# Optimization experiments

Hardware: AMD Instinct MI355X
Metric: run time of the kernel (lower is better)

The kernel has to match this reference:

```python
import jax, jax.numpy as jnp
import numpy as np

M = 256      # num memories in bnn_history
D = 7686     # input_size (2 agent one-hot + 7680 embedding + 4 scalars)
H = 256      # NEAT hidden nodes
O = 4        # NEAT output nodes
N = D + H + O  # total nodes in dense weight matrix


def setup_inputs() -> dict:
    key = jax.random.key(0)
    ks = jax.random.split(key, 8)
    inv_sqrt_d = 1.0 / np.sqrt(D).astype(np.float32)
    return {
        "input_matrix": jax.random.normal(ks[0], (M, D), jnp.float32),
        "Wq": jax.random.normal(ks[1], (D, D), jnp.float32) * inv_sqrt_d,
        "bq": jnp.zeros((D,), jnp.float32),
        "Wk": jax.random.normal(ks[2], (D, D), jnp.float32) * inv_sqrt_d,
        "bk": jnp.zeros((D,), jnp.float32),
        "Wv": jax.random.normal(ks[3], (D, D), jnp.float32) * inv_sqrt_d,
        "bv": jnp.zeros((D,), jnp.float32),
        "weight_mu": jax.random.normal(ks[4], (N, N), jnp.float32) * 0.01,
        "weight_sigma": jnp.full((N, N), 0.1, jnp.float32),  # build_network inits sigma to 0.1
        "bias_mu": jnp.zeros((H + O,), jnp.float32),
        "bias_sigma": jnp.full((H + O,), 0.1, jnp.float32),
        "eps_w": jax.random.normal(ks[5], (N, N), jnp.float32),
        "eps_b": jax.random.normal(ks[6], (H + O,), jnp.float32),
    }


def reference(input_matrix, Wq, bq, Wk, bk, Wv, bv,
              weight_mu, weight_sigma, bias_mu, bias_sigma, eps_w, eps_b):
    # --- attention over memory rows (nn.Linear applies x @ W.T + b) ---
    Q = input_matrix @ Wq.T + bq            # [M, D]
    K = input_matrix @ Wk.T + bk            # [M, D]
    V = input_matrix @ Wv.T + bv            # [M, D]
    scale = 1.0 / jnp.sqrt(jnp.asarray(D, input_matrix.dtype))
    attn = jax.nn.softmax((Q @ K.T) * scale, axis=-1)  # [M, M]
    context = (attn @ V).mean(axis=0)       # [D] pooled attended context

    # --- Bayesian reparameterized genome weights / biases ---
    W = weight_mu + weight_sigma * eps_w    # [N, N], W[i, j] = weight of edge i->j
    b = bias_mu + bias_sigma * eps_b        # [H+O]

    # --- topological NEAT-style evaluation: inputs, then hidden, then outputs ---
    values0 = jnp.zeros((N,), input_matrix.dtype).at[:D].set(context)

    def step(values, j):
        col = jax.lax.dynamic_slice_in_dim(W, j, 1, axis=1)[:, 0]  # incoming weights of node j
        pre = values @ col + b[j - D]        # sum aggregation + bias
        return values.at[j].set(jnp.tanh(pre)), None

    values, _ = jax.lax.scan(step, values0, jnp.arange(D, N))
    return values[-O:]                       # output node activations
```

## Files before the change

### kernel.cpp

```cpp
#include <hip/hip_runtime.h>
#include <hip/hip_bf16.h>
#include <type_traits>

#define DIN   7686
#define NNODE 7946
#define HOUT  260
#define KP    8192

typedef __attribute__((ext_vector_type(8))) short bf16x8;
typedef __attribute__((ext_vector_type(4))) float f32x4;

__device__ __forceinline__ unsigned int f2b(float f) {
  union { float f; unsigned int u; } v; v.f = f;
  return (v.u + 0x7FFFu + ((v.u >> 16) & 1u)) >> 16;
}
__device__ __forceinline__ unsigned int pack2(float lo, float hi) {
  unsigned int r;
  asm("v_cvt_pk_bf16_f32 %0, %1, %2" : "=v"(r) : "v"(lo), "v"(hi));
  return r;
}
__device__ __forceinline__ float b2f(unsigned short h) {
  union { unsigned int u; float f; } v; v.u = ((unsigned int)h) << 16; return v.f;
}
__device__ __forceinline__ void gload16(const void* g, void* l) {
  __builtin_amdgcn_global_load_lds(
      (const __attribute__((address_space(1))) unsigned int*)g,
      (__attribute__((address_space(3))) unsigned int*)l, 16, 0, 0);
}
__device__ __forceinline__ float readlane_f(float v, int lane) {
  return __uint_as_float(__builtin_amdgcn_readlane(__float_as_uint(v), lane));
}

__global__ void prep_x(const float* __restrict__ X, unsigned short* __restrict__ XbT)
{
  const int m = blockIdx.x, t = threadIdx.x;
  const float* row = X + (size_t)m * DIN;
#pragma unroll
  for (int c2 = 0; c2 < 4; ++c2) {
    const int k8 = (c2 * 256 + t) * 8;
    float f[8];
    if (k8 + 8 <= DIN) {
#pragma unroll
      for (int h = 0; h < 4; ++h) {
        float2 v = *(const float2*)(row + k8 + h * 2);
        f[h * 2] = v.x; f[h * 2 + 1] = v.y;
      }
    } else {
#pragma unroll
      for (int h = 0; h < 8; ++h) f[h] = (k8 + h < DIN) ? row[k8 + h] : 0.f;
    }
    uint4 o;
    o.x = pack2(f[0], f[1]); o.y = pack2(f[2], f[3]);
    o.z = pack2(f[4], f[5]); o.w = pack2(f[6], f[7]);
    const int kc = k8 >> 7;
    char* dst = (char*)XbT + (size_t)kc * 65536 + m * 256 +
                (((k8 & 127) * 2) ^ ((m & 7) << 4));
    *(uint4*)dst = o;
  }
}

__global__ __launch_bounds__(512)
void gemm_qk2(const unsigned short* __restrict__ XbT,
              const float* __restrict__ Wq, const float* __restrict__ Wk,
              const float* __restrict__ bq, const float* __restrict__ bk,
              unsigned short* __restrict__ Qbf, unsigned short* __restrict__ Kbf)
{
  const int mat = blockIdx.y;
  const float* W = mat ? Wk : Wq;
  const float* bias = mat ? bk : bq;
  unsigned short* Out = mat ? Kbf : Qbf;
  const int nt = blockIdx.x, n0 = nt * 64;
  const int tid = threadIdx.x, l = tid & 63, wv = tid >> 6;
  const int wr = wv >> 1, wc = wv & 1;
  const int lm = l & 15;

  __shared__ __align__(16) unsigned short As[2][32768];
  __shared__ __align__(16) unsigned short Bs[8192];

  long long wrb[8];
#pragma unroll
  for (int r = 0; r < 8; ++r) {
    int rg = n0 + wv * 8 + r;
    if (rg > DIN - 1) rg = DIN - 1;
    wrb[r] = (long long)rg * DIN;
  }

  float2 breg[8];
  auto RLOADB = [&](int s) {
    const int ss = (s < 64) ? s : 63;
    const int kk = ss * 128 + l * 2;
    const int kcl = (kk < DIN) ? kk : 0;
    const bool ok = kk < DIN;
#pragma unroll
    for (int r = 0; r < 8; ++r) {
      float2 v = *(const float2*)(W + wrb[r] + kcl);
      if (!ok) { v.x = 0.f; v.y = 0.f; }
      breg[r] = v;
    }
  };
  auto SWRITE = [&]() {
#pragma unroll
    for (int r = 0; r < 8; ++r) {
      const int lrow = wv * 8 + r;
      const int off = lrow * 256 + ((l * 4) ^ ((r & 7) << 4));
      *(unsigned int*)((char*)Bs + off) = pack2(breg[r].x, breg[r].y);
    }
  };
  auto GLOADA = [&](int s, int buf) {
    const int kc = (s < 64) ? s : 63;
    const char* g = (const char*)XbT + (size_t)kc * 65536;
    char* lb = (char*)&As[buf][0];
#pragma unroll
    for (int q = 0; q < 8; ++q) {
      const int chunk = q * 8 + wv;
      gload16(g + chunk * 1024 + l * 16, lb + chunk * 1024);
    }
  };

  f32x4 acc[4][2] = {};
  const int sw = (l & 7) << 4;
  const int lq16 = ((l >> 4) & 3) * 16;

  auto COMPUTE = [&](int buf) {
    const char* a_ = (const char*)&As[buf][0];
    const char* b_ = (const char*)Bs;
#pragma unroll
    for (int ks = 0; ks < 4; ++ks) {
      bf16x8 bf[2];
#pragma unroll
      for (int j = 0; j < 2; ++j) {
        const int n = wc * 32 + j * 16 + lm;
        bf[j] = *(const bf16x8*)(b_ + n * 256 + ((ks * 64 + lq16) ^ sw));
      }
#pragma unroll
      for (int i = 0; i < 4; ++i) {
        const int m = wr * 64 + i * 16 + lm;
        bf16x8 a = *(const bf16x8*)(a_ + m * 256 + ((ks * 64 + lq16) ^ sw));
        acc[i][0] = __builtin_amdgcn_mfma_f32_16x16x32_bf16(a, bf[0], acc[i][0], 0, 0, 0);
        acc[i][1] = __builtin_amdgcn_mfma_f32_16x16x32_bf16(a, bf[1], acc[i][1], 0, 0, 0);
      }
    }
  };

#define WAITV(n) { asm volatile("s_waitcnt vmcnt(" #n ")" ::: "memory"); \
                   __builtin_amdgcn_sched_barrier(0); }
#define WAITL    { asm volatile("s_waitcnt lgkmcnt(0)" ::: "memory"); \
                   __builtin_amdgcn_sched_barrier(0); }

  RLOADB(0); GLOADA(0, 0);
  WAITV(0)
  SWRITE();
  RLOADB(1); GLOADA(1, 1);
  WAITL
  __builtin_amdgcn_s_barrier();

  for (int s = 0; s < 64; ++s) {
    COMPUTE(s & 1);
    if (s == 63) break;
    WAITV(8)
    __builtin_amdgcn_s_barrier();
    SWRITE();
    RLOADB(s + 2);
    GLOADA(s + 2, s & 1);
    WAITL
    WAITV(16)
    __builtin_amdgcn_s_barrier();
  }
#undef WAITV
#undef WAITL

#pragma unroll
  for (int i = 0; i < 4; ++i) {
    const int r0 = wr * 64 + i * 16 + (l >> 4) * 4;
#pragma unroll
    for (int j = 0; j < 2; ++j) {
      const int col = n0 + wc * 32 + j * 16 + lm;
      const float bb = (col < DIN) ? bias[col] : 0.f;
#pragma unroll
      for (int q = 0; q < 4; ++q) {
        const float v = acc[i][j][q] + bb;
        Out[(size_t)(r0 + q) * KP + col] = (col < DIN) ? (unsigned short)f2b(v) : 0;
      }
    }
  }
}

__global__ __launch_bounds__(512)
void gemm_logits(const unsigned short* __restrict__ Qbf,
                 const unsigned short* __restrict__ Kbf, float* __restrict__ LP)
{
  const int qr = blockIdx.x & 1, qc = blockIdx.x >> 1, z = blockIdx.z;
  const int tid = threadIdx.x, lane = tid & 63, wv = tid >> 6;
  const int lm = lane & 15, lq = (lane >> 4) * 8;
  const int rowBase = qr * 128 + (wv & 3) * 32;
  const int colBase = qc * 128 + (wv >> 2) * 64;
  const int k0 = z * 128;
  f32x4 acc[2][4] = {};
#pragma unroll
  for (int ks = 0; ks < 4; ++ks) {
    bf16x8 a[2], b[4];
#pragma unroll
    for (int i = 0; i < 2; ++i)
      a[i] = *(const bf16x8*)(Qbf + (size_t)(rowBase + i * 16 + lm) * KP + k0 + ks * 32 + lq);
#pragma unroll
    for (int j = 0; j < 4; ++j)
      b[j] = *(const bf16x8*)(Kbf + (size_t)(colBase + j * 16 + lm) * KP + k0 + ks * 32 + lq);
#pragma unroll
    for (int i = 0; i < 2; ++i)
#pragma unroll
      for (int j = 0; j < 4; ++j)
        acc[i][j] = __builtin_amdgcn_mfma_f32_16x16x32_bf16(a[i], b[j], acc[i][j], 0, 0, 0);
  }
  float* out = LP + (size_t)z * 65536;
#pragma unroll
  for (int i = 0; i < 2; ++i) {
    const int r0 = rowBase + i * 16 + (lane >> 4) * 4;
#pragma unroll
    for (int j = 0; j < 4; ++j) {
      const int col = colBase + j * 16 + lm;
#pragma unroll
      for (int q = 0; q < 4; ++q)
        out[(size_t)(r0 + q) * 256 + col] = acc[i][j][q];
    }
  }
}

__global__ void softmax_fused(const float* __restrict__ LP, float* __restrict__ abar)
{
  __shared__ float red[8];
  const int m = blockIdx.x, t = threadIdx.x;
  float v = 0.f;
#pragma unroll 8
  for (int zz = 0; zz < 64; ++zz) v += LP[(size_t)zz * 65536 + m * 256 + t];
  const float scale = 1.0f / sqrtf((float)DIN);
  float mx = v;
#pragma unroll
  for (int o = 32; o >= 1; o >>= 1) mx = fmaxf(mx, __shfl_xor(mx, o, 64));
  if ((t & 63) == 0) red[t >> 6] = mx;
  __syncthreads();
  mx = fmaxf(fmaxf(red[0], red[1]), fmaxf(red[2], red[3]));
  float e = __expf((v - mx) * scale);
  float s = e;
#pragma unroll
  for (int o = 32; o >= 1; o >>= 1) s += __shfl_xor(s, o, 64);
  if ((t & 63) == 0) red[4 + (t >> 6)] = s;
  __syncthreads();
  s = red[4] + red[5] + red[6] + red[7];
  atomicAdd(&abar[t], e * (1.0f / 256.0f) / s);
}

__global__ void y_kernel(const float* __restrict__ X, const float* __restrict__ abar,
                         float* __restrict__ y)
{
  __shared__ float ab[256];
  ab[threadIdx.x] = abar[threadIdx.x];
  __syncthreads();
  const int c = blockIdx.x * 256 + threadIdx.x;
  if (c >= DIN) return;
  float s = 0.f;
#pragma unroll 8
  for (int m = 0; m < 256; ++m) s += ab[m] * X[(size_t)m * DIN + c];
  y[c] = s;
}

__global__ __launch_bounds__(512)
void ctx_mv(const float* __restrict__ Wv, const float* __restrict__ y,
            const float* __restrict__ bv, float* __restrict__ ctx)
{
  const int wv = threadIdx.x >> 6, l = threadIdx.x & 63;
  const int row = blockIdx.x * 8 + wv;
  if (row >= DIN) return;
  const float* wr_ = Wv + (size_t)row * DIN;
  float s = 0.f;
  for (int it = 0; it < 61; ++it) {
    const int k = it * 128 + l * 2;
    if (k < DIN) {
      float2 w2 = *(const float2*)(wr_ + k);
      float2 y2 = *(const float2*)(y + k);
      s = fmaf(w2.x, y2.x, s);
      s = fmaf(w2.y, y2.y, s);
    }
  }
#pragma unroll
  for (int o = 32; o >= 1; o >>= 1) s += __shfl_xor(s, o, 64);
  if (l == 0) ctx[row] = s + bv[row];
}

__global__ void base_kernel(const float* __restrict__ mu, const float* __restrict__ sg,
                            const float* __restrict__ ep, const float* __restrict__ ctx,
                            float* __restrict__ base)
{
  const int j = threadIdx.x;
  if (j >= HOUT) return;
  const int i0 = blockIdx.x * 31;
  const int i1 = min(i0 + 31, DIN);
  float acc = 0.f;
#pragma unroll 4
  for (int i = i0; i < i1; ++i) {
    const size_t idx = (size_t)i * NNODE + DIN + j;
    acc = fmaf(ctx[i], fmaf(sg[idx], ep[idx], mu[idx]), acc);
  }
  atomicAdd(&base[j], acc);
}

__global__ void ws_kernel(const float* __restrict__ mu, const float* __restrict__ sg,
                          const float* __restrict__ ep, float* __restrict__ WsG)
{
  const int t = blockIdx.x;
  const int j = threadIdx.x;
  if (j >= HOUT) return;
  const size_t idx = (size_t)(DIN + t) * NNODE + DIN + j;
  WsG[t * HOUT + j] = fmaf(sg[idx], ep[idx], mu[idx]);
}

__global__ __launch_bounds__(64, 1)
void scan2(const float* __restrict__ WsG, const float* __restrict__ base,
           const float* __restrict__ bmu, const float* __restrict__ bsg,
           const float* __restrict__ epb, float* __restrict__ out)
{
  __shared__ __align__(16) float tile[32 * HOUT + 128];
  const int l = threadIdx.x;

  float a0, a1, a2, a3, a4;
  {
    int j = l;       a0 = base[j] + bmu[j] + bsg[j] * epb[j];
    j = l + 64;      a1 = base[j] + bmu[j] + bsg[j] * epb[j];
    j = l + 128;     a2 = base[j] + bmu[j] + bsg[j] * epb[j];
    j = l + 192;     a3 = base[j] + bmu[j] + bsg[j] * epb[j];
    j = l + 256;     a4 = (j < HOUT) ? (base[j] + bmu[j] + bsg[j] * epb[j]) : 0.f;
  }

  float4 stg[33];
  auto LOADT = [&](int tb) {
    const int nfl = ((tb == 8) ? 4 : 32) * HOUT;
    const float* src = WsG + tb * 32 * HOUT;
#pragma unroll
    for (int c = 0; c < 33; ++c) {
      const int o = c * 256 + l * 4;
      if (o < nfl) stg[c] = *(const float4*)(src + o);
    }
  };
  auto WRITET = [&](int tb) {
    const int nfl = ((tb == 8) ? 4 : 32) * HOUT;
#pragma unroll
    for (int c = 0; c < 33; ++c) {
      const int o = c * 256 + l * 4;
      if (o < nfl) *(float4*)&tile[o] = stg[c];
    }
  };

  float w0, w1, w2, w3, w4;
  auto PRER = [&](int trow) {
    const float* tr = tile + trow * HOUT;
    w0 = tr[l]; w1 = tr[l + 64]; w2 = tr[l + 128]; w3 = tr[l + 192]; w4 = tr[l + 256];
  };

  auto inner = [&](auto Bc, int tb, int nrows) {
    constexpr int B = Bc.value;
    for (int tt = 0; tt < nrows; ++tt) {
      const int t = tb * 32 + tt;
      float pre;
      if constexpr (B == 0) pre = readlane_f(a0, t & 63);
      else if constexpr (B == 1) pre = readlane_f(a1, t & 63);
      else if constexpr (B == 2) pre = readlane_f(a2, t & 63);
      else if constexpr (B == 3) pre = readlane_f(a3, t & 63);
      else pre = readlane_f(a4, t & 63);
      const float pc = fminf(fmaxf(pre, -12.f), 12.f);
      const float e = __expf(2.f * pc);
      const float vt = 1.f - 2.f / (e + 1.f);
      if (t >= 256 && l == 0) out[t - 256] = vt;
      if (l > t)            a0 = fmaf(vt, w0, a0);
      if (l + 64 > t)       a1 = fmaf(vt, w1, a1);
      if (l + 128 > t)      a2 = fmaf(vt, w2, a2);
      if (l + 192 > t)      a3 = fmaf(vt, w3, a3);
      if (l + 256 > t && l + 256 < HOUT) a4 = fmaf(vt, w4, a4);
      if (tt + 1 < nrows) PRER(tt + 1);
    }
  };

  LOADT(0); WRITET(0); PRER(0);

#define TILE_STEP(tb, B, nr)                                    \
  { if ((tb) < 8) LOADT((tb) + 1);                              \
    inner(std::integral_constant<int, B>{}, (tb), (nr));        \
    if ((tb) < 8) { WRITET((tb) + 1); PRER(0); } }

  TILE_STEP(0, 0, 32)
  TILE_STEP(1, 0, 32)
  TILE_STEP(2, 1, 32)
  TILE_STEP(3, 1, 32)
  TILE_STEP(4, 2, 32)
  TILE_STEP(5, 2, 32)
  TILE_STEP(6, 3, 32)
  TILE_STEP(7, 3, 32)
  TILE_STEP(8, 4, 4)
#undef TILE_STEP
}

extern "C" void kernel_launch(void* const* d_in, const int* in_sizes, int n_in,
                              void* d_out, int out_size, void* d_ws, size_t ws_size,
                              hipStream_t stream)
{
  const float* X   = (const float*)d_in[0];
  const float* Wq  = (const float*)d_in[1];
  const float* bq  = (const float*)d_in[2];
  const float* Wk  = (const float*)d_in[3];
  const float* bk  = (const float*)d_in[4];
  const float* Wv  = (const float*)d_in[5];
  const float* bv  = (const float*)d_in[6];
  const float* wmu = (const float*)d_in[7];
  const float* wsg = (const float*)d_in[8];
  const float* bmu = (const float*)d_in[9];
  const float* bsg = (const float*)d_in[10];
  const float* epw = (const float*)d_in[11];
  const float* epb = (const float*)d_in[12];

  char* p = (char*)d_ws;
  auto alloc = [&](size_t bytes) -> char* {
    char* r = p;
    p += (bytes + 255) & ~(size_t)255;
    return r;
  };
  unsigned short* XbT = (unsigned short*)alloc((size_t)64 * 65536);
  unsigned short* Qbf = (unsigned short*)alloc((size_t)256 * KP * 2);
  unsigned short* Kbf = (unsigned short*)alloc((size_t)256 * KP * 2);
  float* LP   = (float*)alloc((size_t)64 * 65536 * 4);
  float* abar = (float*)alloc(256 * 4);
  float* y    = (float*)alloc(7686 * 4);
  float* ctx  = (float*)alloc(7686 * 4);
  float* base = (float*)alloc(HOUT * 4);
  float* WsG  = (float*)alloc((size_t)HOUT * HOUT * 4 + 1024);

  prep_x<<<dim3(256), dim3(256), 0, stream>>>(X, XbT);
  hipMemsetAsync(abar, 0, 256 * 4, stream);
  hipMemsetAsync(base, 0, HOUT * 4, stream);
  hipMemsetAsync(Qbf, 0, (size_t)256 * KP * 2, stream);
  hipMemsetAsync(Kbf, 0, (size_t)256 * KP * 2, stream);

  gemm_qk2<<<dim3(121, 2), dim3(512), 0, stream>>>(XbT, Wq, Wk, bq, bk, Qbf, Kbf);
  gemm_logits<<<dim3(4, 1, 64), dim3(512), 0, stream>>>(Qbf, Kbf, LP);
  softmax_fused<<<dim3(256), dim3(256), 0, stream>>>(LP, abar);
  y_kernel<<<dim3(31), dim3(256), 0, stream>>>(X, abar, y);
  ctx_mv<<<dim3(961), dim3(512), 0, stream>>>(Wv, y, bv, ctx);
  base_kernel<<<dim3(256), dim3(320), 0, stream>>>(wmu, wsg, epw, ctx, base);
  ws_kernel<<<dim3(260), dim3(320), 0, stream>>>(wmu, wsg, epw, WsG);
  scan2<<<dim3(1), dim3(64), 0, stream>>>(WsG, base, bmu, bsg, epb, (float*)d_out);
}
```

Baseline: 405.7 us.

## Split Q/K projection GEMM along K with register-pipelined B loads and partial reduce

Splits the Q/K projection GEMM into two K halves (grid z=2), so twice as many workgroups stream the large fp32 Wq/Wk matrices, and adds a reduce kernel that sums the bf16 partials and adds the bias. X is prepacked into an MFMA-fragment layout so A operands load straight from global memory into registers. Only B goes through a padded double-buffered LDS tile, with a four-deep register prefetch of W. The cost is extra partial-buffer traffic, an extra launch, and bf16 rounding of the partial sums before reduction.

```diff
diff --git a/kernel.cpp b/kernel.cpp
--- a/kernel.cpp
+++ b/kernel.cpp
@@ -22,19 +22,15 @@
 __device__ __forceinline__ float b2f(unsigned short h) {
   union { unsigned int u; float f; } v; v.u = ((unsigned int)h) << 16; return v.f;
 }
-__device__ __forceinline__ void gload16(const void* g, void* l) {
-  __builtin_amdgcn_global_load_lds(
-      (const __attribute__((address_space(1))) unsigned int*)g,
-      (__attribute__((address_space(3))) unsigned int*)l, 16, 0, 0);
-}
 __device__ __forceinline__ float readlane_f(float v, int lane) {
   return __uint_as_float(__builtin_amdgcn_readlane(__float_as_uint(v), lane));
 }
 
-__global__ void prep_x(const float* __restrict__ X, unsigned short* __restrict__ XbT)
+__global__ void prep_x2(const float* __restrict__ X, char* __restrict__ XbT2)
 {
   const int m = blockIdx.x, t = threadIdx.x;
   const float* row = X + (size_t)m * DIN;
+  const int i16 = m >> 4;
 #pragma unroll
   for (int c2 = 0; c2 < 4; ++c2) {
     const int k8 = (c2 * 256 + t) * 8;
@@ -52,136 +48,144 @@
     uint4 o;
     o.x = pack2(f[0], f[1]); o.y = pack2(f[2], f[3]);
     o.z = pack2(f[4], f[5]); o.w = pack2(f[6], f[7]);
-    const int kc = k8 >> 7;
-    char* dst = (char*)XbT + (size_t)kc * 65536 + m * 256 +
-                (((k8 & 127) * 2) ^ ((m & 7) << 4));
+    const int kc = k8 >> 7, kk = k8 & 127, ks = kk >> 5, hq = (kk & 31) >> 3;
+    const int lane = (m & 15) + (hq << 4);
+    char* dst = XbT2 + ((((size_t)kc * 16 + i16) * 4 + ks) << 10) + lane * 16;
     *(uint4*)dst = o;
   }
 }
 
-__global__ __launch_bounds__(512)
-void gemm_qk2(const unsigned short* __restrict__ XbT,
+__global__ __launch_bounds__(512, 4)
+void gemm_qk3(const char* __restrict__ XbT2,
               const float* __restrict__ Wq, const float* __restrict__ Wk,
-              const float* __restrict__ bq, const float* __restrict__ bk,
-              unsigned short* __restrict__ Qbf, unsigned short* __restrict__ Kbf)
-{
-  const int mat = blockIdx.y;
+              unsigned short* __restrict__ PQK)
+{
+  const int mat = blockIdx.y, z = blockIdx.z;
   const float* W = mat ? Wk : Wq;
-  const float* bias = mat ? bk : bq;
-  unsigned short* Out = mat ? Kbf : Qbf;
-  const int nt = blockIdx.x, n0 = nt * 64;
+  const int n0 = blockIdx.x * 64;
   const int tid = threadIdx.x, l = tid & 63, wv = tid >> 6;
   const int wr = wv >> 1, wc = wv & 1;
-  const int lm = l & 15;
-
-  __shared__ __align__(16) unsigned short As[2][32768];
-  __shared__ __align__(16) unsigned short Bs[8192];
-
-  long long wrb[8];
-#pragma unroll
-  for (int r = 0; r < 8; ++r) {
-    int rg = n0 + wv * 8 + r;
-    if (rg > DIN - 1) rg = DIN - 1;
-    wrb[r] = (long long)rg * DIN;
-  }
-
-  float2 breg[8];
-  auto RLOADB = [&](int s) {
-    const int ss = (s < 64) ? s : 63;
-    const int kk = ss * 128 + l * 2;
-    const int kcl = (kk < DIN) ? kk : 0;
-    const bool ok = kk < DIN;
-#pragma unroll
-    for (int r = 0; r < 8; ++r) {
-      float2 v = *(const float2*)(W + wrb[r] + kcl);
-      if (!ok) { v.x = 0.f; v.y = 0.f; }
-      breg[r] = v;
-    }
-  };
-  auto SWRITE = [&]() {
-#pragma unroll
-    for (int r = 0; r < 8; ++r) {
-      const int lrow = wv * 8 + r;
-      const int off = lrow * 256 + ((l * 4) ^ ((r & 7) << 4));
-      *(unsigned int*)((char*)Bs + off) = pack2(breg[r].x, breg[r].y);
-    }
-  };
-  auto GLOADA = [&](int s, int buf) {
-    const int kc = (s < 64) ? s : 63;
-    const char* g = (const char*)XbT + (size_t)kc * 65536;
-    char* lb = (char*)&As[buf][0];
-#pragma unroll
-    for (int q = 0; q < 8; ++q) {
-      const int chunk = q * 8 + wv;
-      gload16(g + chunk * 1024 + l * 16, lb + chunk * 1024);
-    }
-  };
+  const int lm = l & 15, hq = l >> 4;
+
+  __shared__ __align__(16) char Bs[2][16 * 1040];
+
+  const int br = tid >> 3, q = tid & 7;
+  int bn = n0 + br; if (bn > DIN - 1) bn = DIN - 1;
+  const long long bbase = (long long)bn * DIN;
+  const long long bMax = (long long)DIN * DIN - 2;
+  const int kcBase = z * 32;
+
+  float2 R0[8], R1[8], R2[8], R3[8];
+
+#define LOADB(SET, s) {                                                  \
+    const long long kg = bbase + (long long)(kcBase + (s)) * 128;        \
+    _Pragma("unroll")                                                    \
+    for (int c = 0; c < 2; ++c)                                          \
+      _Pragma("unroll")                                                  \
+      for (int h = 0; h < 4; ++h) {                                      \
+        long long idx = kg + (q + c * 8) * 8 + h * 2;                    \
+        if (idx > bMax) idx = bMax;                                      \
+        SET[c * 4 + h] = *(const float2*)(W + idx);                      \
+      } }
+
+#define SWRITE(buf, SET) {                                               \
+    char* bs_ = Bs[buf];                                                 \
+    _Pragma("unroll")                                                    \
+    for (int c = 0; c < 2; ++c) {                                        \
+      uint4 o_;                                                          \
+      o_.x = pack2(SET[c*4+0].x, SET[c*4+0].y);                          \
+      o_.y = pack2(SET[c*4+1].x, SET[c*4+1].y);                          \
+      o_.z = pack2(SET[c*4+2].x, SET[c*4+2].y);                          \
+      o_.w = pack2(SET[c*4+3].x, SET[c*4+3].y);                          \
+      *(uint4*)(bs_ + (q + c * 8) * 1040 + br * 16) = o_;                \
+    } }
 
   f32x4 acc[4][2] = {};
-  const int sw = (l & 7) << 4;
-  const int lq16 = ((l >> 4) & 3) * 16;
-
-  auto COMPUTE = [&](int buf) {
-    const char* a_ = (const char*)&As[buf][0];
-    const char* b_ = (const char*)Bs;
-#pragma unroll
-    for (int ks = 0; ks < 4; ++ks) {
-      bf16x8 bf[2];
-#pragma unroll
-      for (int j = 0; j < 2; ++j) {
-        const int n = wc * 32 + j * 16 + lm;
-        bf[j] = *(const bf16x8*)(b_ + n * 256 + ((ks * 64 + lq16) ^ sw));
-      }
-#pragma unroll
-      for (int i = 0; i < 4; ++i) {
-        const int m = wr * 64 + i * 16 + lm;
-        bf16x8 a = *(const bf16x8*)(a_ + m * 256 + ((ks * 64 + lq16) ^ sw));
-        acc[i][0] = __builtin_amdgcn_mfma_f32_16x16x32_bf16(a, bf[0], acc[i][0], 0, 0, 0);
-        acc[i][1] = __builtin_amdgcn_mfma_f32_16x16x32_bf16(a, bf[1], acc[i][1], 0, 0, 0);
-      }
-    }
-  };
-
-#define WAITV(n) { asm volatile("s_waitcnt vmcnt(" #n ")" ::: "memory"); \
-                   __builtin_amdgcn_sched_barrier(0); }
-#define WAITL    { asm volatile("s_waitcnt lgkmcnt(0)" ::: "memory"); \
-                   __builtin_amdgcn_sched_barrier(0); }
-
-  RLOADB(0); GLOADA(0, 0);
-  WAITV(0)
-  SWRITE();
-  RLOADB(1); GLOADA(1, 1);
-  WAITL
-  __builtin_amdgcn_s_barrier();
-
-  for (int s = 0; s < 64; ++s) {
-    COMPUTE(s & 1);
-    if (s == 63) break;
-    WAITV(8)
-    __builtin_amdgcn_s_barrier();
-    SWRITE();
-    RLOADB(s + 2);
-    GLOADA(s + 2, s & 1);
-    WAITL
-    WAITV(16)
-    __builtin_amdgcn_s_barrier();
-  }
-#undef WAITV
-#undef WAITL
-
+
+#define COMPUTE(buf, s) {                                                \
+    const int kc_ = kcBase + (s);                                        \
+    bf16x8 a_[4][4];                                                     \
+    _Pragma("unroll")                                                    \
+    for (int i = 0; i < 4; ++i)                                          \
+      _Pragma("unroll")                                                  \
+      for (int ks = 0; ks < 4; ++ks)                                     \
+        a_[i][ks] = *(const bf16x8*)(XbT2 +                              \
+          ((((size_t)kc_ * 16 + (wr * 4 + i)) * 4 + ks) << 10) + l * 16);\
+    const char* bs_ = Bs[buf];                                           \
+    _Pragma("unroll")                                                    \
+    for (int ks = 0; ks < 4; ++ks) {                                     \
+      bf16x8 bf_[2];                                                     \
+      _Pragma("unroll")                                                  \
+      for (int j = 0; j < 2; ++j) {                                      \
+        const int n_ = wc * 32 + j * 16 + lm;                            \
+        bf_[j] = *(const bf16x8*)(bs_ + (ks * 4 + hq) * 1040 + n_ * 16); \
+      }                                                                  \
+      _Pragma("unroll")                                                  \
+      for (int i = 0; i < 4; ++i) {                                      \
+        acc[i][0] = __builtin_amdgcn_mfma_f32_16x16x32_bf16(a_[i][ks], bf_[0], acc[i][0], 0, 0, 0); \
+        acc[i][1] = __builtin_amdgcn_mfma_f32_16x16x32_bf16(a_[i][ks], bf_[1], acc[i][1], 0, 0, 0); \
+      }                                                                  \
+    } }
+
+#define BAR() { asm volatile("s_waitcnt lgkmcnt(0)" ::: "memory");       \
+                __builtin_amdgcn_sched_barrier(0);                       \
+                __builtin_amdgcn_s_barrier();                            \
+                __builtin_amdgcn_sched_barrier(0); }
+
+#define STEP(s, NS) {                                                    \
+    if ((s) + 1 < 32) SWRITE(((s) + 1) & 1, NS)                          \
+    COMPUTE((s) & 1, (s))                                                \
+    if ((s) + 5 < 32) LOADB(NS, (s) + 5)                                 \
+    BAR() }
+
+  LOADB(R0, 0) LOADB(R1, 1) LOADB(R2, 2) LOADB(R3, 3)
+  SWRITE(0, R0)
+  LOADB(R0, 4)
+  BAR()
+
+  for (int su = 0; su < 32; su += 4) {
+    STEP(su + 0, R1)
+    STEP(su + 1, R2)
+    STEP(su + 2, R3)
+    STEP(su + 3, R0)
+  }
+#undef LOADB
+#undef SWRITE
+#undef COMPUTE
+#undef BAR
+#undef STEP
+
+  unsigned short* Cp = PQK + (size_t)(mat * 2 + z) * 256 * KP;
 #pragma unroll
   for (int i = 0; i < 4; ++i) {
     const int r0 = wr * 64 + i * 16 + (l >> 4) * 4;
 #pragma unroll
     for (int j = 0; j < 2; ++j) {
       const int col = n0 + wc * 32 + j * 16 + lm;
-      const float bb = (col < DIN) ? bias[col] : 0.f;
-#pragma unroll
-      for (int q = 0; q < 4; ++q) {
-        const float v = acc[i][j][q] + bb;
-        Out[(size_t)(r0 + q) * KP + col] = (col < DIN) ? (unsigned short)f2b(v) : 0;
-      }
-    }
+#pragma unroll
+      for (int qq = 0; qq < 4; ++qq)
+        Cp[(size_t)(r0 + qq) * KP + col] = (unsigned short)f2b(acc[i][j][qq]);
+    }
+  }
+}
+
+__global__ void reduce_qk3(const unsigned short* __restrict__ PQK,
+                           const float* __restrict__ bq, const float* __restrict__ bk,
+                           unsigned short* __restrict__ Qbf, unsigned short* __restrict__ Kbf)
+{
+  const int mat = blockIdx.y;
+  const int c = blockIdx.x * 128 + threadIdx.x;
+  const float* bias = mat ? bk : bq;
+  const bool valid = c < DIN;
+  const float bb = valid ? bias[c] : 0.f;
+  const unsigned short* P0 = PQK + (size_t)(mat * 2 + 0) * 256 * KP + c;
+  const unsigned short* P1 = PQK + (size_t)(mat * 2 + 1) * 256 * KP + c;
+  unsigned short* O = (mat ? Kbf : Qbf) + c;
+#pragma unroll 4
+  for (int r = 0; r < 256; ++r) {
+    float v = b2f(P0[(size_t)r * KP]) + b2f(P1[(size_t)r * KP]) + bb;
+    if (!valid) v = 0.f;
+    O[(size_t)r * KP] = (unsigned short)f2b(v);
   }
 }
 
@@ -421,7 +425,8 @@
     p += (bytes + 255) & ~(size_t)255;
     return r;
   };
-  unsigned short* XbT = (unsigned short*)alloc((size_t)64 * 65536);
+  char* XbT2 = alloc((size_t)64 * 65536);
+  unsigned short* PQK = (unsigned short*)alloc((size_t)4 * 256 * KP * 2);
   unsigned short* Qbf = (unsigned short*)alloc((size_t)256 * KP * 2);
   unsigned short* Kbf = (unsigned short*)alloc((size_t)256 * KP * 2);
   float* LP   = (float*)alloc((size_t)64 * 65536 * 4);
@@ -431,13 +436,12 @@
   float* base = (float*)alloc(HOUT * 4);
   float* WsG  = (float*)alloc((size_t)HOUT * HOUT * 4 + 1024);
 
-  prep_x<<<dim3(256), dim3(256), 0, stream>>>(X, XbT);
+  prep_x2<<<dim3(256), dim3(256), 0, stream>>>(X, XbT2);
   hipMemsetAsync(abar, 0, 256 * 4, stream);
   hipMemsetAsync(base, 0, HOUT * 4, stream);
-  hipMemsetAsync(Qbf, 0, (size_t)256 * KP * 2, stream);
-  hipMemsetAsync(Kbf, 0, (size_t)256 * KP * 2, stream);
-
-  gemm_qk2<<<dim3(121, 2), dim3(512), 0, stream>>>(XbT, Wq, Wk, bq, bk, Qbf, Kbf);
+
+  gemm_qk3<<<dim3(121, 2, 2), dim3(512), 0, stream>>>(XbT2, Wq, Wk, PQK);
+  reduce_qk3<<<dim3(64, 2), dim3(128), 0, stream>>>(PQK, bq, bk, Qbf, Kbf);
   gemm_logits<<<dim3(4, 1, 64), dim3(512), 0, stream>>>(Qbf, Kbf, LP);
   softmax_fused<<<dim3(256), dim3(256), 0, stream>>>(LP, abar);
   y_kernel<<<dim3(31), dim3(256), 0, stream>>>(X, abar, y);
```

Measured after the change: 480.1 us. 1.18x slower.

## Halve Q/K GEMM tile width, deepen W prefetch pipeline, double-buffer B tiles

Applied to the files above, without the earlier changes.

The Q/K projection GEMM now uses 32-column output tiles with a 64-wide K step, so the grid grows to 241x2 blocks to fill more CUs. It keeps four register sets of W prefetches in flight, double-buffers the B tile in LDS, and adds a launch-bounds occupancy hint. The X staging layout is changed to match the 64-wide K chunks. This targets memory latency on the fp32 weight stream, at the cost of more barriers per byte, repeated A-tile loads across more blocks, and higher register pressure. The ctx matvec loop also gets an unroll pragma.

```diff
diff --git a/kernel.cpp b/kernel.cpp
--- a/kernel.cpp
+++ b/kernel.cpp
@@ -6,6 +6,7 @@
 #define NNODE 7946
 #define HOUT  260
 #define KP    8192
+#define NT    121
 
 typedef __attribute__((ext_vector_type(8))) short bf16x8;
 typedef __attribute__((ext_vector_type(4))) float f32x4;
@@ -19,25 +20,23 @@
   asm("v_cvt_pk_bf16_f32 %0, %1, %2" : "=v"(r) : "v"(lo), "v"(hi));
   return r;
 }
-__device__ __forceinline__ float b2f(unsigned short h) {
-  union { unsigned int u; float f; } v; v.u = ((unsigned int)h) << 16; return v.f;
+__device__ __forceinline__ float readlane_f(float v, int lane) {
+  return __uint_as_float(__builtin_amdgcn_readlane(__float_as_uint(v), lane));
 }
 __device__ __forceinline__ void gload16(const void* g, void* l) {
   __builtin_amdgcn_global_load_lds(
       (const __attribute__((address_space(1))) unsigned int*)g,
       (__attribute__((address_space(3))) unsigned int*)l, 16, 0, 0);
 }
-__device__ __forceinline__ float readlane_f(float v, int lane) {
-  return __uint_as_float(__builtin_amdgcn_readlane(__float_as_uint(v), lane));
-}
-
-__global__ void prep_x(const float* __restrict__ X, unsigned short* __restrict__ XbT)
+
+__global__ void prep_x3(const float* __restrict__ X, char* __restrict__ XbA)
 {
   const int m = blockIdx.x, t = threadIdx.x;
   const float* row = X + (size_t)m * DIN;
 #pragma unroll
   for (int c2 = 0; c2 < 4; ++c2) {
     const int k8 = (c2 * 256 + t) * 8;
+    if (k8 >= NT * 64) continue;
     float f[8];
     if (k8 + 8 <= DIN) {
 #pragma unroll
@@ -52,15 +51,14 @@
     uint4 o;
     o.x = pack2(f[0], f[1]); o.y = pack2(f[2], f[3]);
     o.z = pack2(f[4], f[5]); o.w = pack2(f[6], f[7]);
-    const int kc = k8 >> 7;
-    char* dst = (char*)XbT + (size_t)kc * 65536 + m * 256 +
-                (((k8 & 127) * 2) ^ ((m & 7) << 4));
+    const int kc = k8 >> 6, kf = k8 & 63;
+    char* dst = XbA + (size_t)kc * 32768 + m * 128 + ((kf * 2) ^ ((m & 7) << 4));
     *(uint4*)dst = o;
   }
 }
 
-__global__ __launch_bounds__(512)
-void gemm_qk2(const unsigned short* __restrict__ XbT,
+__global__ __launch_bounds__(512, 4)
+void gemm_qk4(const char* __restrict__ XbA,
               const float* __restrict__ Wq, const float* __restrict__ Wk,
               const float* __restrict__ bq, const float* __restrict__ bk,
               unsigned short* __restrict__ Qbf, unsigned short* __restrict__ Kbf)
@@ -69,118 +67,114 @@
   const float* W = mat ? Wk : Wq;
   const float* bias = mat ? bk : bq;
   unsigned short* Out = mat ? Kbf : Qbf;
-  const int nt = blockIdx.x, n0 = nt * 64;
+  const int n0 = blockIdx.x * 32;
   const int tid = threadIdx.x, l = tid & 63, wv = tid >> 6;
   const int wr = wv >> 1, wc = wv & 1;
-  const int lm = l & 15;
-
-  __shared__ __align__(16) unsigned short As[2][32768];
-  __shared__ __align__(16) unsigned short Bs[8192];
-
-  long long wrb[8];
-#pragma unroll
-  for (int r = 0; r < 8; ++r) {
-    int rg = n0 + wv * 8 + r;
-    if (rg > DIN - 1) rg = DIN - 1;
-    wrb[r] = (long long)rg * DIN;
-  }
-
-  float2 breg[8];
-  auto RLOADB = [&](int s) {
-    const int ss = (s < 64) ? s : 63;
-    const int kk = ss * 128 + l * 2;
-    const int kcl = (kk < DIN) ? kk : 0;
-    const bool ok = kk < DIN;
-#pragma unroll
-    for (int r = 0; r < 8; ++r) {
-      float2 v = *(const float2*)(W + wrb[r] + kcl);
-      if (!ok) { v.x = 0.f; v.y = 0.f; }
-      breg[r] = v;
-    }
-  };
-  auto SWRITE = [&]() {
-#pragma unroll
-    for (int r = 0; r < 8; ++r) {
-      const int lrow = wv * 8 + r;
-      const int off = lrow * 256 + ((l * 4) ^ ((r & 7) << 4));
-      *(unsigned int*)((char*)Bs + off) = pack2(breg[r].x, breg[r].y);
-    }
-  };
-  auto GLOADA = [&](int s, int buf) {
-    const int kc = (s < 64) ? s : 63;
-    const char* g = (const char*)XbT + (size_t)kc * 65536;
-    char* lb = (char*)&As[buf][0];
-#pragma unroll
-    for (int q = 0; q < 8; ++q) {
-      const int chunk = q * 8 + wv;
-      gload16(g + chunk * 1024 + l * 16, lb + chunk * 1024);
-    }
-  };
-
-  f32x4 acc[4][2] = {};
-  const int sw = (l & 7) << 4;
-  const int lq16 = ((l >> 4) & 3) * 16;
-
-  auto COMPUTE = [&](int buf) {
-    const char* a_ = (const char*)&As[buf][0];
-    const char* b_ = (const char*)Bs;
-#pragma unroll
-    for (int ks = 0; ks < 4; ++ks) {
-      bf16x8 bf[2];
-#pragma unroll
-      for (int j = 0; j < 2; ++j) {
-        const int n = wc * 32 + j * 16 + lm;
-        bf[j] = *(const bf16x8*)(b_ + n * 256 + ((ks * 64 + lq16) ^ sw));
-      }
-#pragma unroll
-      for (int i = 0; i < 4; ++i) {
-        const int m = wr * 64 + i * 16 + lm;
-        bf16x8 a = *(const bf16x8*)(a_ + m * 256 + ((ks * 64 + lq16) ^ sw));
-        acc[i][0] = __builtin_amdgcn_mfma_f32_16x16x32_bf16(a, bf[0], acc[i][0], 0, 0, 0);
-        acc[i][1] = __builtin_amdgcn_mfma_f32_16x16x32_bf16(a, bf[1], acc[i][1], 0, 0, 0);
-      }
-    }
-  };
-
-#define WAITV(n) { asm volatile("s_waitcnt vmcnt(" #n ")" ::: "memory"); \
-                   __builtin_amdgcn_sched_barrier(0); }
-#define WAITL    { asm volatile("s_waitcnt lgkmcnt(0)" ::: "memory"); \
-                   __builtin_amdgcn_sched_barrier(0); }
-
-  RLOADB(0); GLOADA(0, 0);
-  WAITV(0)
-  SWRITE();
-  RLOADB(1); GLOADA(1, 1);
-  WAITL
-  __builtin_amdgcn_s_barrier();
-
-  for (int s = 0; s < 64; ++s) {
-    COMPUTE(s & 1);
-    if (s == 63) break;
-    WAITV(8)
-    __builtin_amdgcn_s_barrier();
-    SWRITE();
-    RLOADB(s + 2);
-    GLOADA(s + 2, s & 1);
-    WAITL
-    WAITV(16)
-    __builtin_amdgcn_s_barrier();
-  }
+  const int lm = l & 15, hq = l >> 4;
+
+  __shared__ __align__(16) char Abuf[2][32768];
+  __shared__ __align__(16) char Bbuf[2][4096];
+
+  const int brow = tid >> 4, kq = tid & 15;
+  const int bn = min(n0 + brow, DIN - 1);
+  const long long bbase = (long long)bn * DIN;
+  const long long DD = (long long)DIN * DIN;
+
+  float4 S0, S1, S2, S3;
+
+#define LOADB(SET, t_) {                                                  \
+    const int kc_ = min((t_), NT - 1);                                    \
+    long long idx_ = bbase + kc_ * 64 + kq * 4;                           \
+    if (idx_ + 4 <= DD) SET = *(const float4*)(W + idx_);                 \
+    else { float4 tt_ = *(const float4*)(W + DD - 4);                     \
+           SET.x = tt_.z; SET.y = tt_.w; SET.z = 0.f; SET.w = 0.f; } }
+
+#define SWRITE(buf, SET) {                                                \
+    unsigned long long pk_ = (unsigned long long)pack2(SET.x, SET.y) |    \
+                     ((unsigned long long)pack2(SET.z, SET.w) << 32);     \
+    *(unsigned long long*)(Bbuf[buf] + brow * 128 +                       \
+        ((kq * 8) ^ ((brow & 7) << 4))) = pk_; }
+
+#define GA(t_, buf) {                                                     \
+    const int kc_ = min((t_), NT - 1);                                    \
+    const char* g_ = XbA + (size_t)kc_ * 32768;                           \
+    char* lb_ = Abuf[buf];                                                \
+    _Pragma("unroll")                                                     \
+    for (int q_ = 0; q_ < 4; ++q_) {                                      \
+      const int ch_ = q_ * 8 + wv;                                        \
+      gload16(g_ + ch_ * 1024 + l * 16, lb_ + ch_ * 1024);                \
+    } }
+
+  f32x4 acc[4] = {};
+
+#define COMPUTE(buf) {                                                    \
+    const char* a_ = Abuf[buf];                                           \
+    const char* b_ = Bbuf[buf];                                           \
+    _Pragma("unroll")                                                     \
+    for (int ks_ = 0; ks_ < 2; ++ks_) {                                   \
+      const int nl_ = wc * 16 + lm;                                       \
+      bf16x8 bf_ = *(const bf16x8*)(b_ + nl_ * 128 +                      \
+          (((ks_ * 64 + hq * 16)) ^ ((nl_ & 7) << 4)));                   \
+      _Pragma("unroll")                                                   \
+      for (int i_ = 0; i_ < 4; ++i_) {                                    \
+        const int m_ = wr * 64 + i_ * 16 + lm;                            \
+        bf16x8 af_ = *(const bf16x8*)(a_ + m_ * 128 +                     \
+            (((ks_ * 64 + hq * 16)) ^ ((m_ & 7) << 4)));                  \
+        acc[i_] = __builtin_amdgcn_mfma_f32_16x16x32_bf16(af_, bf_, acc[i_], 0, 0, 0); \
+      }                                                                   \
+    } }
+
+#define SB()     __builtin_amdgcn_sched_barrier(0)
+#define WAITV(n) { asm volatile("s_waitcnt vmcnt(" #n ")" ::: "memory"); SB(); }
+#define WAITL()  { asm volatile("s_waitcnt lgkmcnt(0)" ::: "memory"); SB(); }
+
+  LOADB(S0, 0) LOADB(S1, 1) LOADB(S2, 2) LOADB(S3, 3)
+  GA(0, 0)
+  WAITV(7)
+  SWRITE(0, S0)
+  LOADB(S0, 4)
+  GA(1, 1)
+  WAITV(5)
+  WAITL()
+  __builtin_amdgcn_s_barrier(); SB();
+
+#define STEP(s_, CS) {                                                    \
+    WAITV(11)                                                             \
+    if ((s_) + 1 < NT) SWRITE(((s_) + 1) & 1, CS)                         \
+    LOADB(CS, (s_) + 5)                                                   \
+    SB();                                                                 \
+    COMPUTE((s_) & 1)                                                     \
+    WAITV(1)                                                              \
+    WAITL()                                                               \
+    __builtin_amdgcn_s_barrier(); SB();                                   \
+    if ((s_) + 2 < NT) GA((s_) + 2, (s_) & 1)                             \
+  }
+
+  for (int su = 0; su < NT - 1; su += 4) {
+    STEP(su + 0, S1)
+    STEP(su + 1, S2)
+    STEP(su + 2, S3)
+    STEP(su + 3, S0)
+  }
+  STEP(NT - 1, S1)
+#undef STEP
+#undef LOADB
+#undef SWRITE
+#undef GA
+#undef COMPUTE
 #undef WAITV
 #undef WAITL
+#undef SB
 
 #pragma unroll
   for (int i = 0; i < 4; ++i) {
     const int r0 = wr * 64 + i * 16 + (l >> 4) * 4;
-#pragma unroll
-    for (int j = 0; j < 2; ++j) {
-      const int col = n0 + wc * 32 + j * 16 + lm;
-      const float bb = (col < DIN) ? bias[col] : 0.f;
-#pragma unroll
-      for (int q = 0; q < 4; ++q) {
-        const float v = acc[i][j][q] + bb;
-        Out[(size_t)(r0 + q) * KP + col] = (col < DIN) ? (unsigned short)f2b(v) : 0;
-      }
+    const int col = n0 + wc * 16 + lm;
+    const float bb = (col < DIN) ? bias[col] : 0.f;
+#pragma unroll
+    for (int q = 0; q < 4; ++q) {
+      const float v = acc[i][q] + bb;
+      Out[(size_t)(r0 + q) * KP + col] = (col < DIN) ? (unsigned short)f2b(v) : 0;
     }
   }
 }
@@ -272,6 +266,7 @@
   if (row >= DIN) return;
   const float* wr_ = Wv + (size_t)row * DIN;
   float s = 0.f;
+#pragma unroll 4
   for (int it = 0; it < 61; ++it) {
     const int k = it * 128 + l * 2;
     if (k < DIN) {
@@ -421,7 +416,7 @@
     p += (bytes + 255) & ~(size_t)255;
     return r;
   };
-  unsigned short* XbT = (unsigned short*)alloc((size_t)64 * 65536);
+  char* XbA = alloc((size_t)NT * 32768);
   unsigned short* Qbf = (unsigned short*)alloc((size_t)256 * KP * 2);
   unsigned short* Kbf = (unsigned short*)alloc((size_t)256 * KP * 2);
   float* LP   = (float*)alloc((size_t)64 * 65536 * 4);
@@ -431,13 +426,13 @@
   float* base = (float*)alloc(HOUT * 4);
   float* WsG  = (float*)alloc((size_t)HOUT * HOUT * 4 + 1024);
 
-  prep_x<<<dim3(256), dim3(256), 0, stream>>>(X, XbT);
+  prep_x3<<<dim3(256), dim3(256), 0, stream>>>(X, XbA);
   hipMemsetAsync(abar, 0, 256 * 4, stream);
   hipMemsetAsync(base, 0, HOUT * 4, stream);
   hipMemsetAsync(Qbf, 0, (size_t)256 * KP * 2, stream);
   hipMemsetAsync(Kbf, 0, (size_t)256 * KP * 2, stream);
 
-  gemm_qk2<<<dim3(121, 2), dim3(512), 0, stream>>>(XbT, Wq, Wk, bq, bk, Qbf, Kbf);
+  gemm_qk4<<<dim3(241, 2), dim3(512), 0, stream>>>(XbA, Wq, Wk, bq, bk, Qbf, Kbf);
   gemm_logits<<<dim3(4, 1, 64), dim3(512), 0, stream>>>(Qbf, Kbf, LP);
   softmax_fused<<<dim3(256), dim3(256), 0, stream>>>(LP, abar);
   y_kernel<<<dim3(31), dim3(256), 0, stream>>>(X, abar, y);
```

Result: slower. 449.3 us (+10.8%).
